# Kernel optimization log

Hardware: AMD Instinct MI355X
Metric: run time of the kernel (lower is better)

Reference implementation:

```python
import jax, jax.numpy as jnp
import numpy as np

NUM_CLASSES = 5
LOSS_WEIGHT = 1.0
EPS_CENTER = 1e-6   # torch code's +1e-06 in the masked mean
EPS_COS = 1e-8      # torch nn.CosineSimilarity default eps


def _nearest_idx(out_size, in_size):
    # PyTorch nn.Upsample(mode='nearest'): in_idx = floor(out_idx * in/out)
    return (jnp.arange(out_size) * in_size) // out_size


def _upsample_labels(target, D, H, W):
    # target: [B,1,d,h,w] int labels -> [B,D,H,W]
    lab = target[:, 0]
    d, h, w = lab.shape[1], lab.shape[2], lab.shape[3]
    lab = lab[:, _nearest_idx(D, d)]
    lab = lab[:, :, _nearest_idx(H, h)]
    lab = lab[:, :, :, _nearest_idx(W, w)]
    return lab


def _per_voxel_centers(feat, onehot, labf, counts):
    # feat: [B,C,V], onehot: [B,V,K], labf: [B,V], counts: [B,K]
    sums = jnp.einsum('bcv,bvk->bck', feat, onehot)          # [B,C,K]
    means = sums / (counts[:, None, :] + EPS_CENTER)          # [B,C,K]
    # broadcast class mean back to every voxel of that class
    centers = jnp.take_along_axis(means, labf[:, None, :], axis=2)  # [B,C,V]
    if NUM_CLASSES == 2:
        # original code skips class 0 when num_classes == 2
        centers = jnp.where(labf[:, None, :] == 0, feat, centers)
    return centers


def _cosine(a, b):
    # cosine similarity along channel dim (axis=1), torch semantics
    dot = jnp.sum(a * b, axis=1)
    na = jnp.sqrt(jnp.sum(a * a, axis=1))
    nb = jnp.sqrt(jnp.sum(b * b, axis=1))
    return dot / jnp.maximum(na * nb, EPS_COS)


def reference(feat_S, feat_T, target):
    B, C, D, H, W = feat_S.shape
    V = D * H * W
    labf = _upsample_labels(target, D, H, W).reshape(B, V)    # [B,V]
    onehot = jax.nn.one_hot(labf, NUM_CLASSES, dtype=feat_S.dtype)  # [B,V,K]
    counts = onehot.sum(axis=1)                                # [B,K]

    fS = feat_S.reshape(B, C, V)
    fT = feat_T.reshape(B, C, V)
    centerS = _per_voxel_centers(fS, onehot, labf, counts)
    centerT = _per_voxel_centers(fT, onehot, labf, counts)

    pcsim_S = _cosine(fS, centerS)   # [B,V]
    pcsim_T = _cosine(fT, centerT)   # [B,V]
    loss = jnp.mean((pcsim_S - pcsim_T) ** 2)
    return LOSS_WEIGHT * loss


def setup_inputs() -> dict:
    key = jax.random.key(0)
    k1, k2, k3 = jax.random.split(key, 3)
    feat_S = jax.random.normal(k1, (2, 64, 32, 64, 64), dtype=jnp.float32)
    feat_T = jax.random.normal(k2, (2, 64, 32, 64, 64), dtype=jnp.float32)
    target = jax.random.randint(k3, (2, 1, 16, 32, 32), 0, NUM_CLASSES, dtype=jnp.int32)
    return {"feat_S": feat_S, "feat_T": feat_T, "target": target}
```

## Files before the change

### kernel.cpp

```cpp
#include <hip/hip_runtime.h>
#include <math.h>

#define NUM_CLASSES 5
constexpr int B = 2, C = 64, D = 32, H = 64, W = 64;
constexpr int V = D * H * W;
constexpr int TD = 16, TH = 32, TW = 32;
constexpr int TVOX = TD * TH * TW;
constexpr float EPS_CENTER = 1e-6f;
constexpr float EPS_COS = 1e-8f;

typedef float f32x4 __attribute__((ext_vector_type(4)));
typedef float f32x2 __attribute__((ext_vector_type(2)));

constexpr int OFF_SUMS_S = 0;
constexpr int OFF_SUMS_T = 640;
constexpr int OFF_LOSS   = 1280;
constexpr int OFF_TICKET = 1281;
constexpr int OFF_CNT    = 1284;
constexpr int WS_FLOATS  = 1312;

__device__ __forceinline__ f32x4 ntload4(const float* p) {
    return __builtin_nontemporal_load(reinterpret_cast<const f32x4*>(p));
}
__device__ __forceinline__ f32x2 ntload2(const float* p) {
    return __builtin_nontemporal_load(reinterpret_cast<const f32x2*>(p));
}

__global__ void prep_kernel(const int* __restrict__ tgt, float* __restrict__ ws) {
    __shared__ int wred[4][NUM_CLASSES];
    const int tid = threadIdx.x;
    const int bid = blockIdx.x;
    if (bid < B) {
        int cnt[NUM_CLASSES] = {0, 0, 0, 0, 0};
        const int4* tp = reinterpret_cast<const int4*>(tgt + bid * TVOX);
#pragma unroll
        for (int i = 0; i < 16; ++i) {
            int4 v = tp[tid + i * 256];
#pragma unroll
            for (int k = 0; k < NUM_CLASSES; ++k)
                cnt[k] += (v.x == k) + (v.y == k) + (v.z == k) + (v.w == k);
        }
        int lane = tid & 63, wid = tid >> 6;
#pragma unroll
        for (int k = 0; k < NUM_CLASSES; ++k) {
            int v = cnt[k];
            for (int off = 32; off; off >>= 1) v += __shfl_down(v, off);
            if (lane == 0) wred[wid][k] = v;
        }
        __syncthreads();
        if (tid < NUM_CLASSES)
            ws[OFF_CNT + bid * NUM_CLASSES + tid] =
                8.0f * (float)(wred[0][tid] + wred[1][tid] + wred[2][tid] + wred[3][tid]);
    } else {
        int i = (bid - B) * 256 + tid;
        if (i < OFF_TICKET + 1) ws[i] = 0.0f;
    }
}

__global__ __launch_bounds__(512, 4) void sums_kernel(
    const float* __restrict__ fS, const float* __restrict__ fT,
    const int* __restrict__ tgt, float* __restrict__ ws)
{
    const int bc = blockIdx.y;
    const int b = bc >> 6, c = bc & 63;
    const int q = blockIdx.x;
    const int tid = threadIdx.x;

    float accS[NUM_CLASSES] = {0, 0, 0, 0, 0};
    float accT[NUM_CLASSES] = {0, 0, 0, 0, 0};

#pragma unroll
    for (int it = 0; it < 4; ++it) {
        const int* tb = tgt + b * TVOX + (q * 4 + it) * (TH * TW) + (tid & 15) * 2;
        int2 L0 = *reinterpret_cast<const int2*>(tb + (tid >> 5) * TW);
        int2 L1 = *reinterpret_cast<const int2*>(tb + (16 + (tid >> 5)) * TW);

        const long base = (long)bc * V + q * 32768 + it * 8192 + tid * 4;
        f32x4 s0 = ntload4(fS + base);
        f32x4 s1 = ntload4(fS + base + 2048);
        f32x4 s2 = ntload4(fS + base + 4096);
        f32x4 s3 = ntload4(fS + base + 6144);
        f32x4 t0 = ntload4(fT + base);
        f32x4 t1 = ntload4(fT + base + 2048);
        f32x4 t2 = ntload4(fT + base + 4096);
        f32x4 t3 = ntload4(fT + base + 6144);

        float sA01 = (s0.x + s0.y) + (s2.x + s2.y), sA23 = (s0.z + s0.w) + (s2.z + s2.w);
        float sB01 = (s1.x + s1.y) + (s3.x + s3.y), sB23 = (s1.z + s1.w) + (s3.z + s3.w);
        float tA01 = (t0.x + t0.y) + (t2.x + t2.y), tA23 = (t0.z + t0.w) + (t2.z + t2.w);
        float tB01 = (t1.x + t1.y) + (t3.x + t3.y), tB23 = (t1.z + t1.w) + (t3.z + t3.w);
#pragma unroll
        for (int k = 0; k < NUM_CLASSES; ++k) {
            accS[k] += ((L0.x == k) ? sA01 : 0.0f) + ((L0.y == k) ? sA23 : 0.0f)
                     + ((L1.x == k) ? sB01 : 0.0f) + ((L1.y == k) ? sB23 : 0.0f);
            accT[k] += ((L0.x == k) ? tA01 : 0.0f) + ((L0.y == k) ? tA23 : 0.0f)
                     + ((L1.x == k) ? tB01 : 0.0f) + ((L1.y == k) ? tB23 : 0.0f);
        }
    }

    __shared__ float wsum[8][2 * NUM_CLASSES];
    int lane = tid & 63, wid = tid >> 6;
#pragma unroll
    for (int k = 0; k < NUM_CLASSES; ++k) {
        float vS = accS[k], vT = accT[k];
        for (int off = 32; off; off >>= 1) {
            vS += __shfl_down(vS, off);
            vT += __shfl_down(vT, off);
        }
        if (lane == 0) { wsum[wid][k] = vS; wsum[wid][NUM_CLASSES + k] = vT; }
    }
    __syncthreads();
    if (tid < 2 * NUM_CLASSES) {
        float v = 0.0f;
#pragma unroll
        for (int w = 0; w < 8; ++w) v += wsum[w][tid];
        int k = tid % NUM_CLASSES;
        int dst = ((tid < NUM_CLASSES) ? OFF_SUMS_S : OFF_SUMS_T) + (b * NUM_CLASSES + k) * C + c;
        atomicAdd(&ws[dst], v);
    }
}

__global__ __launch_bounds__(512) void loss_kernel(
    const float* __restrict__ fS, const float* __restrict__ fT,
    const int* __restrict__ tgt, float* __restrict__ ws, float* __restrict__ out)
{
    __shared__ float mST[C * NUM_CLASSES * 2];
    __shared__ float nrm[2][8];
    __shared__ float red[8];
    int tid = threadIdx.x;
    int b = blockIdx.y;

    for (int i = tid; i < C * NUM_CLASSES; i += 512) {
        int c = i / NUM_CLASSES, k = i % NUM_CLASSES;
        float cnt = ws[OFF_CNT + b * NUM_CLASSES + k] + EPS_CENTER;
        mST[i * 2]     = ws[OFF_SUMS_S + (b * NUM_CLASSES + k) * C + c] / cnt;
        mST[i * 2 + 1] = ws[OFF_SUMS_T + (b * NUM_CLASSES + k) * C + c] / cnt;
    }
    __syncthreads();
    if (tid < 2 * NUM_CLASSES) {
        int k = tid % NUM_CLASSES;
        int st = tid / NUM_CLASSES;
        float s = 0.0f;
        for (int c = 0; c < C; ++c) { float v = mST[(c * NUM_CLASSES + k) * 2 + st]; s += v * v; }
        nrm[st][k] = sqrtf(s);
    }
    __syncthreads();

    int v = blockIdx.x * 1024 + tid * 2;
    int z = v >> 12, y = (v >> 6) & 63, x = v & 63;
    int k = tgt[b * TVOX + (z >> 1) * (TH * TW) + (y >> 1) * TW + (x >> 1)];

    const float* pS = fS + (long)b * C * V + v;
    const float* pT = fT + (long)b * C * V + v;
    float d0S = 0, d1S = 0, q0S = 0, q1S = 0;
    float d0T = 0, d1T = 0, q0T = 0, q1T = 0;

    for (int cb = 0; cb < C; cb += 8) {
        f32x2 a[8], t[8];
#pragma unroll
        for (int j = 0; j < 8; ++j) a[j] = ntload2(pS + (long)(cb + j) * V);
#pragma unroll
        for (int j = 0; j < 8; ++j) t[j] = ntload2(pT + (long)(cb + j) * V);
#pragma unroll
        for (int j = 0; j < 8; ++j) {
            float2 m = *reinterpret_cast<const float2*>(&mST[((cb + j) * NUM_CLASSES + k) * 2]);
            d0S += a[j].x * m.x; d1S += a[j].y * m.x;
            q0S += a[j].x * a[j].x; q1S += a[j].y * a[j].y;
            d0T += t[j].x * m.y; d1T += t[j].y * m.y;
            q0T += t[j].x * t[j].x; q1T += t[j].y * t[j].y;
        }
    }

    float c0S = d0S / fmaxf(sqrtf(q0S) * nrm[0][k], EPS_COS);
    float c1S = d1S / fmaxf(sqrtf(q1S) * nrm[0][k], EPS_COS);
    float c0T = d0T / fmaxf(sqrtf(q0T) * nrm[1][k], EPS_COS);
    float c1T = d1T / fmaxf(sqrtf(q1T) * nrm[1][k], EPS_COS);
    float e0 = c0S - c0T, e1 = c1S - c1T;
    float val = e0 * e0 + e1 * e1;

    for (int off = 32; off; off >>= 1) val += __shfl_down(val, off);
    int lane = tid & 63, wid = tid >> 6;
    if (lane == 0) red[wid] = val;
    __syncthreads();
    if (tid == 0) {
        float blk = 0.0f;
#pragma unroll
        for (int w = 0; w < 8; ++w) blk += red[w];
        atomicAdd(&ws[OFF_LOSS], blk);
        __threadfence();
        int prev = atomicAdd(reinterpret_cast<int*>(ws) + OFF_TICKET, 1);
        if (prev == (int)(gridDim.x * gridDim.y) - 1) {
            float total = atomicAdd(&ws[OFF_LOSS], 0.0f);
            out[0] = total * (1.0f / (float)(B * V));
        }
    }
}

extern "C" void kernel_launch(void* const* d_in, const int* in_sizes, int n_in,
                              void* d_out, int out_size, void* d_ws, size_t ws_size,
                              hipStream_t stream) {
    const float* fS  = (const float*)d_in[0];
    const float* fT  = (const float*)d_in[1];
    const int*   tgt = (const int*)d_in[2];
    float* out = (float*)d_out;
    float* ws  = (float*)d_ws;

    prep_kernel<<<dim3(B + 6), 256, 0, stream>>>(tgt, ws);
    sums_kernel<<<dim3(4, B * C), 512, 0, stream>>>(fS, fT, tgt, ws);
    loss_kernel<<<dim3(V / 1024, B), 512, 0, stream>>>(fS, fT, tgt, ws, out);
}
```

Measured before the change: 58.46 us.

## Drop label-count prep kernel using cosine scale invariance and per-quarter partial sums

Removes the prep kernel that counted labels per class and zeroed the workspace. Cosine similarity does not change when a class center is scaled by a positive factor, so the raw class sums can stand in for the class means. The sums kernel now writes per-quarter partial sums to separate slots instead of using atomics, and it also zeroes the loss and ticket words. The loss kernel adds the four partials together. This saves one launch and the atomic traffic. The trade-off is a small numeric difference near the EPS_COS clamp, since norms are no longer divided by the count.

```diff
diff --git a/kernel.cpp b/kernel.cpp
--- a/kernel.cpp
+++ b/kernel.cpp
@@ -6,55 +6,22 @@
 constexpr int V = D * H * W;
 constexpr int TD = 16, TH = 32, TW = 32;
 constexpr int TVOX = TD * TH * TW;
-constexpr float EPS_CENTER = 1e-6f;
 constexpr float EPS_COS = 1e-8f;
 
 typedef float f32x4 __attribute__((ext_vector_type(4)));
 typedef float f32x2 __attribute__((ext_vector_type(2)));
 
 constexpr int OFF_SUMS_S = 0;
-constexpr int OFF_SUMS_T = 640;
-constexpr int OFF_LOSS   = 1280;
-constexpr int OFF_TICKET = 1281;
-constexpr int OFF_CNT    = 1284;
-constexpr int WS_FLOATS  = 1312;
+constexpr int OFF_SUMS_T = 2560;
+constexpr int OFF_LOSS   = 5120;
+constexpr int OFF_TICKET = 5121;
+constexpr int WS_FLOATS  = 5136;
 
 __device__ __forceinline__ f32x4 ntload4(const float* p) {
     return __builtin_nontemporal_load(reinterpret_cast<const f32x4*>(p));
 }
 __device__ __forceinline__ f32x2 ntload2(const float* p) {
     return __builtin_nontemporal_load(reinterpret_cast<const f32x2*>(p));
-}
-
-__global__ void prep_kernel(const int* __restrict__ tgt, float* __restrict__ ws) {
-    __shared__ int wred[4][NUM_CLASSES];
-    const int tid = threadIdx.x;
-    const int bid = blockIdx.x;
-    if (bid < B) {
-        int cnt[NUM_CLASSES] = {0, 0, 0, 0, 0};
-        const int4* tp = reinterpret_cast<const int4*>(tgt + bid * TVOX);
-#pragma unroll
-        for (int i = 0; i < 16; ++i) {
-            int4 v = tp[tid + i * 256];
-#pragma unroll
-            for (int k = 0; k < NUM_CLASSES; ++k)
-                cnt[k] += (v.x == k) + (v.y == k) + (v.z == k) + (v.w == k);
-        }
-        int lane = tid & 63, wid = tid >> 6;
-#pragma unroll
-        for (int k = 0; k < NUM_CLASSES; ++k) {
-            int v = cnt[k];
-            for (int off = 32; off; off >>= 1) v += __shfl_down(v, off);
-            if (lane == 0) wred[wid][k] = v;
-        }
-        __syncthreads();
-        if (tid < NUM_CLASSES)
-            ws[OFF_CNT + bid * NUM_CLASSES + tid] =
-                8.0f * (float)(wred[0][tid] + wred[1][tid] + wred[2][tid] + wred[3][tid]);
-    } else {
-        int i = (bid - B) * 256 + tid;
-        if (i < OFF_TICKET + 1) ws[i] = 0.0f;
-    }
 }
 
 __global__ __launch_bounds__(512, 4) void sums_kernel(
@@ -115,9 +82,11 @@
 #pragma unroll
         for (int w = 0; w < 8; ++w) v += wsum[w][tid];
         int k = tid % NUM_CLASSES;
-        int dst = ((tid < NUM_CLASSES) ? OFF_SUMS_S : OFF_SUMS_T) + (b * NUM_CLASSES + k) * C + c;
-        atomicAdd(&ws[dst], v);
+        int base = (tid < NUM_CLASSES) ? OFF_SUMS_S : OFF_SUMS_T;
+        ws[base + ((b * NUM_CLASSES + k) * C + c) * 4 + q] = v;
     }
+    if (q == 0 && bc == 0 && tid >= 2 * NUM_CLASSES && tid < 2 * NUM_CLASSES + 2)
+        ws[OFF_LOSS + (tid - 2 * NUM_CLASSES)] = 0.0f;
 }
 
 __global__ __launch_bounds__(512) void loss_kernel(
@@ -132,9 +101,15 @@
 
     for (int i = tid; i < C * NUM_CLASSES; i += 512) {
         int c = i / NUM_CLASSES, k = i % NUM_CLASSES;
-        float cnt = ws[OFF_CNT + b * NUM_CLASSES + k] + EPS_CENTER;
-        mST[i * 2]     = ws[OFF_SUMS_S + (b * NUM_CLASSES + k) * C + c] / cnt;
-        mST[i * 2 + 1] = ws[OFF_SUMS_T + (b * NUM_CLASSES + k) * C + c] / cnt;
+        int wi = ((b * NUM_CLASSES + k) * C + c) * 4;
+        float sS = 0.0f, sT = 0.0f;
+#pragma unroll
+        for (int qq = 0; qq < 4; ++qq) {
+            sS += ws[OFF_SUMS_S + wi + qq];
+            sT += ws[OFF_SUMS_T + wi + qq];
+        }
+        mST[i * 2]     = sS;
+        mST[i * 2 + 1] = sT;
     }
     __syncthreads();
     if (tid < 2 * NUM_CLASSES) {
@@ -205,7 +180,6 @@
     float* out = (float*)d_out;
     float* ws  = (float*)d_ws;
 
-    prep_kernel<<<dim3(B + 6), 256, 0, stream>>>(tgt, ws);
     sums_kernel<<<dim3(4, B * C), 512, 0, stream>>>(fS, fT, tgt, ws);
     loss_kernel<<<dim3(V / 1024, B), 512, 0, stream>>>(fS, fT, tgt, ws, out);
 }
```

Result: faster. 55.08 us (-5.8%).
